# Performance work log

Measured on AMD Instinct MI355X. Metric: run time of the kernel, lower is better.

Reference implementation:

```python
import jax, jax.numpy as jnp
import numpy as np

B, N, C, H = 16, 4096, 1024, 8
D = C // H  # head dim = 128
EPS = 1e-5


def layernorm(x, gamma, beta):
    mu = jnp.mean(x, axis=-1, keepdims=True)
    var = jnp.mean(jnp.square(x - mu), axis=-1, keepdims=True)
    return (x - mu) * jax.lax.rsqrt(var + EPS) * gamma + beta


def setup_inputs() -> dict:
    key = jax.random.key(0)
    ks = jax.random.split(key, 5)
    w_std = C ** -0.5
    return {
        "class_feature": jax.random.normal(ks[0], (1, 1, C), dtype=jnp.float32),
        "features": jax.random.normal(ks[1], (B, N, C), dtype=jnp.float32),
        "q_gamma": jnp.ones((C,), jnp.float32),
        "q_beta": jnp.zeros((C,), jnp.float32),
        "Wq": jax.random.normal(ks[2], (C, C), dtype=jnp.float32) * w_std,
        "kv_gamma": jnp.ones((C,), jnp.float32),
        "kv_beta": jnp.zeros((C,), jnp.float32),
        "Wkv": jax.random.normal(ks[3], (2 * C, C), dtype=jnp.float32) * w_std,
        "proj_W": jax.random.normal(ks[4], (C, C), dtype=jnp.float32) * w_std,
        "proj_b": jnp.zeros((C,), jnp.float32),
    }


def reference(class_feature, features, q_gamma, q_beta, Wq,
              kv_gamma, kv_beta, Wkv, proj_W, proj_b):
    b, n, c = features.shape
    scale = c ** -0.5  # NOTE: original scales by input_size^-0.5, not head_dim^-0.5
    cf = jnp.broadcast_to(class_feature, (b, 1, c))  # repeat(B,1,1)

    # q branch: LN + Linear (no bias); single query token per batch
    q = layernorm(cf, q_gamma, q_beta) @ Wq.T            # (B,1,C)
    q = q.reshape(b, H, D)                               # (B,H,D)

    # kv branch: LN + Linear -> split into k,v per head
    kv = layernorm(features, kv_gamma, kv_beta) @ Wkv.T  # (B,N,2C)
    kv = kv.reshape(b, n, 2, H, D)
    k = kv[:, :, 0]                                      # (B,N,H,D)
    v = kv[:, :, 1]                                      # (B,N,H,D)

    # single-query attention per head
    attn = jnp.einsum('bhd,bnhd->bhn', q * scale, k)     # (B,H,N)
    attn = jax.nn.softmax(attn, axis=-1)
    agg = jnp.einsum('bhn,bnhd->bhd', attn, v)           # (B,H,D)
    agg = agg.reshape(b, 1, c)

    return cf + agg @ proj_W.T + proj_b
```

## Files before the change

### kernel.cpp

```cpp
#include <hip/hip_runtime.h>
#include <math.h>


#define BB 16
#define NN 4096
#define CC 1024
#define HH 8
#define DD 128
#define CHUNKS 64
#define RPB 64
#define TPT 4
#define NT 16

constexpr float EPS_ = 1e-5f;
constexpr float SCALE_ = 0.03125f;

__device__ __forceinline__ float wsum(float v) {
#pragma unroll
  for (int o = 32; o; o >>= 1) v += __shfl_xor(v, o, 64);
  return v;
}

__device__ __forceinline__ float dpp_sum63(float v) {
  int t;
  t = __builtin_amdgcn_update_dpp(0, __float_as_int(v), 0x111, 0xf, 0xf, true);  v += __int_as_float(t);
  t = __builtin_amdgcn_update_dpp(0, __float_as_int(v), 0x112, 0xf, 0xf, true);  v += __int_as_float(t);
  t = __builtin_amdgcn_update_dpp(0, __float_as_int(v), 0x114, 0xf, 0xf, true);  v += __int_as_float(t);
  t = __builtin_amdgcn_update_dpp(0, __float_as_int(v), 0x118, 0xf, 0xf, true);  v += __int_as_float(t);
  t = __builtin_amdgcn_update_dpp(0, __float_as_int(v), 0x142, 0xa, 0xf, false); v += __int_as_float(t);
  t = __builtin_amdgcn_update_dpp(0, __float_as_int(v), 0x143, 0xc, 0xf, false); v += __int_as_float(t);
  return v;
}

__device__ __forceinline__ float rsum_u(float v) {
  return __int_as_float(__builtin_amdgcn_readlane(__float_as_int(dpp_sum63(v)), 63));
}

__device__ __forceinline__ float dot4(const float4& a, const float4& b) {
  return a.x * b.x + a.y * b.y + a.z * b.z + a.w * b.w;
}
__device__ __forceinline__ void fma4(float4& a, float s, const float4& v) {
  a.x += s * v.x; a.y += s * v.y; a.z += s * v.z; a.w += s * v.w;
}

__device__ __forceinline__ void bar_lgkm() {
  asm volatile("s_waitcnt lgkmcnt(0)" ::: "memory");
  __builtin_amdgcn_sched_barrier(0);
  __builtin_amdgcn_s_barrier();
  __builtin_amdgcn_sched_barrier(0);
}

__global__ __launch_bounds__(256) void k0b(const float* __restrict__ cf,
                                           const float* __restrict__ g,
                                           const float* __restrict__ be,
                                           const float* __restrict__ Wq,
                                           float* __restrict__ qvec) {
  __shared__ __align__(16) float lnbuf[CC];
  __shared__ float red[8];
  int t = threadIdx.x, lane = t & 63, wid = t >> 6;
  float x[4];
  float s = 0.f, s2 = 0.f;
#pragma unroll
  for (int j = 0; j < 4; ++j) {
    x[j] = cf[t * 4 + j];
    s += x[j];
    s2 += x[j] * x[j];
  }
  s = wsum(s);
  s2 = wsum(s2);
  if (lane == 0) { red[wid] = s; red[4 + wid] = s2; }
  __syncthreads();
  float S = red[0] + red[1] + red[2] + red[3];
  float S2 = red[4] + red[5] + red[6] + red[7];
  float mu = S * (1.f / CC);
  float rstd = rsqrtf(S2 * (1.f / CC) - mu * mu + EPS_);
#pragma unroll
  for (int j = 0; j < 4; ++j)
    lnbuf[t * 4 + j] = (x[j] - mu) * rstd * g[t * 4 + j] + be[t * 4 + j];
  __syncthreads();
  int j = blockIdx.x * 4 + wid;
  const float4* wr = (const float4*)(Wq + (size_t)j * CC);
  const float4* l4 = (const float4*)lnbuf;
  float a = 0.f;
#pragma unroll
  for (int k = 0; k < 4; ++k) a += dot4(wr[lane + 64 * k], l4[lane + 64 * k]);
  a = wsum(a);
  if (lane == 0) qvec[j] = a;
}

__global__ __launch_bounds__(256) void k0c(const float* __restrict__ qvec,
                                           const float* __restrict__ Wkv,
                                           const float* __restrict__ kvg,
                                           float* __restrict__ qW,
                                           float* __restrict__ qWg) {
  int h = blockIdx.x >> 4;
  int c0 = (blockIdx.x & 15) * 64;
  int t = threadIdx.x, cl = t & 63, g = t >> 6;
  float a = 0.f;
#pragma unroll 8
  for (int d = g * 32; d < g * 32 + 32; ++d)
    a += qvec[h * DD + d] * Wkv[((size_t)(h * DD + d)) * CC + c0 + cl];
  __shared__ float red[4][64];
  red[g][cl] = a;
  __syncthreads();
  if (t < 64) {
    float v = (red[0][t] + red[1][t] + red[2][t] + red[3][t]) * SCALE_;
    qW[h * CC + c0 + t] = v;
    qWg[h * CC + c0 + t] = v * kvg[c0 + t];
  }
}

__global__ __launch_bounds__(256, 2) void kfused(
    const float* __restrict__ x, const float* __restrict__ qWg,
    const float* __restrict__ qW, const float* __restrict__ kvb,
    float* __restrict__ part_s, float* __restrict__ part_meu) {
  __shared__ __align__(16) float xbuf[2][TPT * CC];
  __shared__ __align__(8) float mr_lds[2][TPT][2];

  const int t = threadIdx.x, lane = t & 63, wid = t >> 6;
  const int chunk = blockIdx.x, b = blockIdx.y;
  const int bc = b * CHUNKS + chunk;
  const int h0 = wid * 2;

  const float* gx = x + ((size_t)b * NN + (size_t)chunk * RPB) * CC;
  const int sl = wid * 256 + lane;

  float4 pf[4];
  {
    const float4* g0 = (const float4*)gx;
#pragma unroll
    for (int k = 0; k < 4; ++k) pf[k] = g0[sl + 64 * k];
  }

  float4 qw0[4], qw1[4];
  {
    const float4* a0 = (const float4*)(qWg + (size_t)h0 * CC);
    const float4* a1 = (const float4*)(qWg + (size_t)(h0 + 1) * CC);
#pragma unroll
    for (int k = 0; k < 4; ++k) {
      qw0[k] = a0[lane + 64 * k];
      qw1[k] = a1[lane + 64 * k];
    }
  }
  float qs0, qs1, qb0, qb1;
  {
    float s0 = 0.f, s1 = 0.f, t0 = 0.f, t1 = 0.f;
    const float4* w0 = (const float4*)(qW + (size_t)h0 * CC);
    const float4* w1 = (const float4*)(qW + (size_t)(h0 + 1) * CC);
    const float4* b4 = (const float4*)kvb;
#pragma unroll
    for (int k = 0; k < 4; ++k) {
      s0 += qw0[k].x + qw0[k].y + qw0[k].z + qw0[k].w;
      s1 += qw1[k].x + qw1[k].y + qw1[k].z + qw1[k].w;
      float4 bt = b4[lane + 64 * k];
      t0 += dot4(w0[lane + 64 * k], bt);
      t1 += dot4(w1[lane + 64 * k], bt);
    }
    qs0 = rsum_u(s0);
    qs1 = rsum_u(s1);
    qb0 = rsum_u(t0);
    qb1 = rsum_u(t1);
  }

  float4 acc0[4], acc1[4];
#pragma unroll
  for (int k = 0; k < 4; ++k) {
    acc0[k] = make_float4(0.f, 0.f, 0.f, 0.f);
    acc1[k] = make_float4(0.f, 0.f, 0.f, 0.f);
  }
  float e0 = 0.f, e1 = 0.f, un0 = 0.f, un1 = 0.f;

  for (int tl = 0; tl < NT; ++tl) {
    const int cur = tl & 1;
    float ls = 0.f, ls2 = 0.f;
#pragma unroll
    for (int k = 0; k < 4; ++k) {
      ls += pf[k].x + pf[k].y + pf[k].z + pf[k].w;
      ls2 += dot4(pf[k], pf[k]);
    }
    {
      float4* dst = (float4*)xbuf[cur];
#pragma unroll
      for (int k = 0; k < 4; ++k) dst[sl + 64 * k] = pf[k];
    }
    ls = dpp_sum63(ls);
    ls2 = dpp_sum63(ls2);
    if (lane == 63) {
      float mu = ls * (1.f / CC);
      float rs = rsqrtf(ls2 * (1.f / CC) - mu * mu + EPS_);
      mr_lds[cur][wid][0] = mu;
      mr_lds[cur][wid][1] = rs;
    }
    if (tl + 1 < NT) {
      const float4* gn = (const float4*)(gx + (size_t)(tl + 1) * (TPT * CC));
#pragma unroll
      for (int k = 0; k < 4; ++k) pf[k] = gn[sl + 64 * k];
    }
    bar_lgkm();

    const float4* xb4 = (const float4*)xbuf[cur];
#pragma unroll
    for (int r = 0; r < TPT; ++r) {
      float4 x0 = xb4[r * 256 + lane];
      float4 x1 = xb4[r * 256 + lane + 64];
      float4 x2 = xb4[r * 256 + lane + 128];
      float4 x3 = xb4[r * 256 + lane + 192];
      float a0 = dot4(qw0[0], x0), a1 = dot4(qw0[1], x1);
      float a2 = dot4(qw0[2], x2), a3 = dot4(qw0[3], x3);
      float c0 = dot4(qw1[0], x0), c1 = dot4(qw1[1], x1);
      float c2 = dot4(qw1[2], x2), c3 = dot4(qw1[3], x3);
      float D0 = rsum_u((a0 + a1) + (a2 + a3));
      float D1 = rsum_u((c0 + c1) + (c2 + c3));
      float2 mr = *(const float2*)mr_lds[cur][r];
      float mu = mr.x, rs = mr.y;
      float l0 = fminf(rs * (D0 - mu * qs0) + qb0, 75.f);
      float l1 = fminf(rs * (D1 - mu * qs1) + qb1, 75.f);
      float p0 = __expf(l0), p1 = __expf(l1);
      float w0 = p0 * rs, w1 = p1 * rs;
      e0 += p0; e1 += p1;
      un0 += w0 * mu; un1 += w1 * mu;
      fma4(acc0[0], w0, x0); fma4(acc0[1], w0, x1);
      fma4(acc0[2], w0, x2); fma4(acc0[3], w0, x3);
      fma4(acc1[0], w1, x0); fma4(acc1[1], w1, x1);
      fma4(acc1[2], w1, x2); fma4(acc1[3], w1, x3);
    }
  }

  float4* p0 = (float4*)(part_s + ((size_t)bc * HH + h0) * CC);
  float4* p1 = (float4*)(part_s + ((size_t)bc * HH + h0 + 1) * CC);
#pragma unroll
  for (int k = 0; k < 4; ++k) {
    p0[64 * k + lane] = acc0[k];
    p1[64 * k + lane] = acc1[k];
  }
  if (lane == 0) {
    float* pm = part_meu + ((size_t)bc * HH + h0) * 3;
    pm[0] = 0.f; pm[1] = e0; pm[2] = un0;
    pm[3] = 0.f; pm[4] = e1; pm[5] = un1;
  }
}

__global__ __launch_bounds__(256) void kmerge(
    const float* __restrict__ part_s, const float* __restrict__ part_meu,
    const float* __restrict__ kvg, const float* __restrict__ kvb,
    float* __restrict__ s) {
  int h = blockIdx.x >> 2, q = blockIdx.x & 3, b = blockIdx.y;
  int col = q * 256 + threadIdx.x;
  float E = 0.f, UN = 0.f, a = 0.f;
  for (int ch = 0; ch < CHUNKS; ++ch) {
    const float* pm = part_meu + (((size_t)b * CHUNKS + ch) * HH + h) * 3;
    E += pm[1];
    UN += pm[2];
    a += part_s[(((size_t)b * CHUNKS + ch) * HH + h) * CC + col];
  }
  float inv = 1.f / E;
  s[((size_t)b * HH + h) * CC + col] = kvg[col] * (a - UN) * inv + kvb[col];
}

__global__ __launch_bounds__(256) void k5(const float* __restrict__ Wkv,
                                          const float* __restrict__ s,
                                          float* __restrict__ agg) {
  int lane = threadIdx.x & 63;
  int j = blockIdx.x * 4 + (threadIdx.x >> 6);
  int h = j >> 7;
  const float4* wr = (const float4*)(Wkv + ((size_t)(CC + j)) * CC);
  float4 wv[4];
#pragma unroll
  for (int k = 0; k < 4; ++k) wv[k] = wr[lane + 64 * k];
  for (int b = 0; b < BB; ++b) {
    const float4* s4 = (const float4*)(s + ((size_t)(b * HH + h)) * CC);
    float a = 0.f;
#pragma unroll
    for (int k = 0; k < 4; ++k) a += dot4(wv[k], s4[lane + 64 * k]);
    a = wsum(a);
    if (lane == 0) agg[b * CC + j] = a;
  }
}

__global__ __launch_bounds__(256) void k6(const float* __restrict__ pW,
                                          const float* __restrict__ agg,
                                          const float* __restrict__ cf,
                                          const float* __restrict__ pb,
                                          float* __restrict__ out) {
  int lane = threadIdx.x & 63;
  int j = blockIdx.x * 4 + (threadIdx.x >> 6);
  const float4* wr = (const float4*)(pW + (size_t)j * CC);
  float4 wv[4];
#pragma unroll
  for (int k = 0; k < 4; ++k) wv[k] = wr[lane + 64 * k];
  for (int b = 0; b < BB; ++b) {
    const float4* a4 = (const float4*)(agg + (size_t)b * CC);
    float a = 0.f;
#pragma unroll
    for (int k = 0; k < 4; ++k) a += dot4(wv[k], a4[lane + 64 * k]);
    a = wsum(a);
    if (lane == 0) out[b * CC + j] = cf[j] + a + pb[j];
  }
}

constexpr size_t WS_QVEC = 0;
constexpr size_t WS_QW   = 1024;
constexpr size_t WS_QWG  = 9216;
constexpr size_t WS_S    = 17408;
constexpr size_t WS_AGG  = 148480;
constexpr size_t WS_PMEU = 164864;
constexpr size_t WS_PART = 189440;

extern "C" void kernel_launch(void* const* d_in, const int* in_sizes, int n_in,
                              void* d_out, int out_size, void* d_ws, size_t ws_size,
                              hipStream_t stream) {
  const float* cf = (const float*)d_in[0];
  const float* x = (const float*)d_in[1];
  const float* qg = (const float*)d_in[2];
  const float* qb = (const float*)d_in[3];
  const float* Wq = (const float*)d_in[4];
  const float* kvg = (const float*)d_in[5];
  const float* kvb = (const float*)d_in[6];
  const float* Wkv = (const float*)d_in[7];
  const float* pW = (const float*)d_in[8];
  const float* pb = (const float*)d_in[9];
  float* ws = (float*)d_ws;
  float* out = (float*)d_out;

  k0b<<<256, 256, 0, stream>>>(cf, qg, qb, Wq, ws + WS_QVEC);
  k0c<<<128, 256, 0, stream>>>(ws + WS_QVEC, Wkv, kvg, ws + WS_QW, ws + WS_QWG);
  kfused<<<dim3(CHUNKS, BB), 256, 0, stream>>>(x, ws + WS_QWG, ws + WS_QW, kvb,
                                               ws + WS_PART, ws + WS_PMEU);
  kmerge<<<dim3(HH * 4, BB), 256, 0, stream>>>(ws + WS_PART, ws + WS_PMEU, kvg, kvb,
                                               ws + WS_S);
  k5<<<256, 256, 0, stream>>>(Wkv, ws + WS_S, ws + WS_AGG);
  k6<<<256, 256, 0, stream>>>(pW, ws + WS_AGG, cf, pb, out);
}
```

Baseline: 114.1 us.

## Double rows per tile in fused kernel, halving chunk count and partials

Raises rows per tile from 4 to 8 so each wave loads and normalizes two rows per iteration. Halving the chunk count halves the partial sums written and merged, and the per-chunk meta record shrinks from three floats to two. The larger shared tile (64KB per block) and the doubled prefetch registers may cut occupancy. Halving the block count (512 blocks) can also leave CUs underused.

```diff
diff --git a/kernel.cpp b/kernel.cpp
--- a/kernel.cpp
+++ b/kernel.cpp
@@ -7,9 +7,9 @@
 #define CC 1024
 #define HH 8
 #define DD 128
-#define CHUNKS 64
-#define RPB 64
-#define TPT 4
+#define CHUNKS 32
+#define RPB 128
+#define TPT 8
 #define NT 16
 
 constexpr float EPS_ = 1e-5f;
@@ -38,6 +38,9 @@
 
 __device__ __forceinline__ float dot4(const float4& a, const float4& b) {
   return a.x * b.x + a.y * b.y + a.z * b.z + a.w * b.w;
+}
+__device__ __forceinline__ float sum4(const float4& a) {
+  return (a.x + a.y) + (a.z + a.w);
 }
 __device__ __forceinline__ void fma4(float4& a, float s, const float4& v) {
   a.x += s * v.x; a.y += s * v.y; a.z += s * v.z; a.w += s * v.w;
@@ -121,15 +124,18 @@
   const int chunk = blockIdx.x, b = blockIdx.y;
   const int bc = b * CHUNKS + chunk;
   const int h0 = wid * 2;
+  const int ra = wid * 2, rb = ra + 1;
 
   const float* gx = x + ((size_t)b * NN + (size_t)chunk * RPB) * CC;
-  const int sl = wid * 256 + lane;
-
-  float4 pf[4];
+
+  float4 pf[8];
   {
     const float4* g0 = (const float4*)gx;
 #pragma unroll
-    for (int k = 0; k < 4; ++k) pf[k] = g0[sl + 64 * k];
+    for (int k = 0; k < 4; ++k) {
+      pf[k] = g0[ra * 256 + lane + 64 * k];
+      pf[4 + k] = g0[rb * 256 + lane + 64 * k];
+    }
   }
 
   float4 qw0[4], qw1[4];
@@ -150,8 +156,8 @@
     const float4* b4 = (const float4*)kvb;
 #pragma unroll
     for (int k = 0; k < 4; ++k) {
-      s0 += qw0[k].x + qw0[k].y + qw0[k].z + qw0[k].w;
-      s1 += qw1[k].x + qw1[k].y + qw1[k].z + qw1[k].w;
+      s0 += sum4(qw0[k]);
+      s1 += sum4(qw1[k]);
       float4 bt = b4[lane + 64 * k];
       t0 += dot4(w0[lane + 64 * k], bt);
       t1 += dot4(w1[lane + 64 * k], bt);
@@ -172,29 +178,44 @@
 
   for (int tl = 0; tl < NT; ++tl) {
     const int cur = tl & 1;
-    float ls = 0.f, ls2 = 0.f;
+
+    float lsA = 0.f, lsA2 = 0.f, lsB = 0.f, lsB2 = 0.f;
 #pragma unroll
     for (int k = 0; k < 4; ++k) {
-      ls += pf[k].x + pf[k].y + pf[k].z + pf[k].w;
-      ls2 += dot4(pf[k], pf[k]);
+      lsA += sum4(pf[k]);
+      lsA2 += dot4(pf[k], pf[k]);
+      lsB += sum4(pf[4 + k]);
+      lsB2 += dot4(pf[4 + k], pf[4 + k]);
     }
     {
       float4* dst = (float4*)xbuf[cur];
 #pragma unroll
-      for (int k = 0; k < 4; ++k) dst[sl + 64 * k] = pf[k];
-    }
-    ls = dpp_sum63(ls);
-    ls2 = dpp_sum63(ls2);
+      for (int k = 0; k < 4; ++k) {
+        dst[ra * 256 + lane + 64 * k] = pf[k];
+        dst[rb * 256 + lane + 64 * k] = pf[4 + k];
+      }
+    }
+    lsA = dpp_sum63(lsA);
+    lsA2 = dpp_sum63(lsA2);
+    lsB = dpp_sum63(lsB);
+    lsB2 = dpp_sum63(lsB2);
     if (lane == 63) {
-      float mu = ls * (1.f / CC);
-      float rs = rsqrtf(ls2 * (1.f / CC) - mu * mu + EPS_);
-      mr_lds[cur][wid][0] = mu;
-      mr_lds[cur][wid][1] = rs;
+      float muA = lsA * (1.f / CC);
+      float rsA = rsqrtf(lsA2 * (1.f / CC) - muA * muA + EPS_);
+      float muB = lsB * (1.f / CC);
+      float rsB = rsqrtf(lsB2 * (1.f / CC) - muB * muB + EPS_);
+      mr_lds[cur][ra][0] = muA;
+      mr_lds[cur][ra][1] = rsA;
+      mr_lds[cur][rb][0] = muB;
+      mr_lds[cur][rb][1] = rsB;
     }
     if (tl + 1 < NT) {
       const float4* gn = (const float4*)(gx + (size_t)(tl + 1) * (TPT * CC));
 #pragma unroll
-      for (int k = 0; k < 4; ++k) pf[k] = gn[sl + 64 * k];
+      for (int k = 0; k < 4; ++k) {
+        pf[k] = gn[ra * 256 + lane + 64 * k];
+        pf[4 + k] = gn[rb * 256 + lane + 64 * k];
+      }
     }
     bar_lgkm();
 
@@ -234,9 +255,9 @@
     p1[64 * k + lane] = acc1[k];
   }
   if (lane == 0) {
-    float* pm = part_meu + ((size_t)bc * HH + h0) * 3;
-    pm[0] = 0.f; pm[1] = e0; pm[2] = un0;
-    pm[3] = 0.f; pm[4] = e1; pm[5] = un1;
+    float* pm = part_meu + ((size_t)bc * HH + h0) * 2;
+    pm[0] = e0; pm[1] = un0;
+    pm[2] = e1; pm[3] = un1;
   }
 }
 
@@ -248,9 +269,9 @@
   int col = q * 256 + threadIdx.x;
   float E = 0.f, UN = 0.f, a = 0.f;
   for (int ch = 0; ch < CHUNKS; ++ch) {
-    const float* pm = part_meu + (((size_t)b * CHUNKS + ch) * HH + h) * 3;
-    E += pm[1];
-    UN += pm[2];
+    const float* pm = part_meu + (((size_t)b * CHUNKS + ch) * HH + h) * 2;
+    E += pm[0];
+    UN += pm[1];
     a += part_s[(((size_t)b * CHUNKS + ch) * HH + h) * CC + col];
   }
   float inv = 1.f / E;
@@ -304,7 +325,7 @@
 constexpr size_t WS_S    = 17408;
 constexpr size_t WS_AGG  = 148480;
 constexpr size_t WS_PMEU = 164864;
-constexpr size_t WS_PART = 189440;
+constexpr size_t WS_PART = 173056;
 
 extern "C" void kernel_launch(void* const* d_in, const int* in_sizes, int n_in,
                               void* d_out, int out_size, void* d_ws, size_t ws_size,
```

Result: slower. 229.9 us (+101.5%).

## Use packed FP32 FMAs in attention loop and halve chunk count

Applied to the files above, without the earlier changes.

The main streaming kernel now does its dot products, LayerNorm statistics and weighted accumulation with v_pk_fma_f32/v_pk_add_f32 inline asm on float pairs, which is meant to halve the VALU instruction count per row. Rows per block double and the chunk count halves, so there are fewer partial results for the merge kernel to reduce. The per-chunk metadata also drops from three floats to two. The cost is fewer blocks in flight, less latency hiding, and inline asm that limits compiler scheduling.

```diff
diff --git a/kernel.cpp b/kernel.cpp
--- a/kernel.cpp
+++ b/kernel.cpp
@@ -7,13 +7,24 @@
 #define CC 1024
 #define HH 8
 #define DD 128
-#define CHUNKS 64
-#define RPB 64
+#define CHUNKS 32
+#define RPB 128
 #define TPT 4
-#define NT 16
+#define NT 32
 
 constexpr float EPS_ = 1e-5f;
 constexpr float SCALE_ = 0.03125f;
+
+typedef float v2f __attribute__((ext_vector_type(2)));
+
+__device__ __forceinline__ void pkfma(v2f& d, v2f a, v2f b) {
+  asm("v_pk_fma_f32 %0, %1, %2, %0" : "+v"(d) : "v"(a), "v"(b));
+}
+__device__ __forceinline__ void pkadd(v2f& d, v2f a) {
+  asm("v_pk_add_f32 %0, %1, %0" : "+v"(d) : "v"(a));
+}
+__device__ __forceinline__ v2f lo2(const float4& f) { return v2f{f.x, f.y}; }
+__device__ __forceinline__ v2f hi2(const float4& f) { return v2f{f.z, f.w}; }
 
 __device__ __forceinline__ float wsum(float v) {
 #pragma unroll
@@ -39,8 +50,8 @@
 __device__ __forceinline__ float dot4(const float4& a, const float4& b) {
   return a.x * b.x + a.y * b.y + a.z * b.z + a.w * b.w;
 }
-__device__ __forceinline__ void fma4(float4& a, float s, const float4& v) {
-  a.x += s * v.x; a.y += s * v.y; a.z += s * v.z; a.w += s * v.w;
+__device__ __forceinline__ float sum4(const float4& a) {
+  return (a.x + a.y) + (a.z + a.w);
 }
 
 __device__ __forceinline__ void bar_lgkm() {
@@ -150,8 +161,8 @@
     const float4* b4 = (const float4*)kvb;
 #pragma unroll
     for (int k = 0; k < 4; ++k) {
-      s0 += qw0[k].x + qw0[k].y + qw0[k].z + qw0[k].w;
-      s1 += qw1[k].x + qw1[k].y + qw1[k].z + qw1[k].w;
+      s0 += sum4(qw0[k]);
+      s1 += sum4(qw1[k]);
       float4 bt = b4[lane + 64 * k];
       t0 += dot4(w0[lane + 64 * k], bt);
       t1 += dot4(w1[lane + 64 * k], bt);
@@ -162,34 +173,41 @@
     qb1 = rsum_u(t1);
   }
 
-  float4 acc0[4], acc1[4];
-#pragma unroll
-  for (int k = 0; k < 4; ++k) {
-    acc0[k] = make_float4(0.f, 0.f, 0.f, 0.f);
-    acc1[k] = make_float4(0.f, 0.f, 0.f, 0.f);
+  v2f acc0[8], acc1[8];
+#pragma unroll
+  for (int k = 0; k < 8; ++k) {
+    acc0[k] = v2f{0.f, 0.f};
+    acc1[k] = v2f{0.f, 0.f};
   }
   float e0 = 0.f, e1 = 0.f, un0 = 0.f, un1 = 0.f;
 
   for (int tl = 0; tl < NT; ++tl) {
     const int cur = tl & 1;
-    float ls = 0.f, ls2 = 0.f;
-#pragma unroll
-    for (int k = 0; k < 4; ++k) {
-      ls += pf[k].x + pf[k].y + pf[k].z + pf[k].w;
-      ls2 += dot4(pf[k], pf[k]);
-    }
     {
-      float4* dst = (float4*)xbuf[cur];
-#pragma unroll
-      for (int k = 0; k < 4; ++k) dst[sl + 64 * k] = pf[k];
-    }
-    ls = dpp_sum63(ls);
-    ls2 = dpp_sum63(ls2);
-    if (lane == 63) {
-      float mu = ls * (1.f / CC);
-      float rs = rsqrtf(ls2 * (1.f / CC) - mu * mu + EPS_);
-      mr_lds[cur][wid][0] = mu;
-      mr_lds[cur][wid][1] = rs;
+      v2f sv = v2f{0.f, 0.f}, sv2 = v2f{0.f, 0.f};
+#pragma unroll
+      for (int k = 0; k < 4; ++k) {
+        v2f plo = lo2(pf[k]), phi = hi2(pf[k]);
+        pkadd(sv, plo);
+        pkadd(sv, phi);
+        pkfma(sv2, plo, plo);
+        pkfma(sv2, phi, phi);
+      }
+      float ls = sv.x + sv.y;
+      float ls2 = sv2.x + sv2.y;
+      {
+        float4* dst = (float4*)xbuf[cur];
+#pragma unroll
+        for (int k = 0; k < 4; ++k) dst[sl + 64 * k] = pf[k];
+      }
+      ls = dpp_sum63(ls);
+      ls2 = dpp_sum63(ls2);
+      if (lane == 63) {
+        float mu = ls * (1.f / CC);
+        float rs = rsqrtf(ls2 * (1.f / CC) - mu * mu + EPS_);
+        mr_lds[cur][wid][0] = mu;
+        mr_lds[cur][wid][1] = rs;
+      }
     }
     if (tl + 1 < NT) {
       const float4* gn = (const float4*)(gx + (size_t)(tl + 1) * (TPT * CC));
@@ -205,12 +223,19 @@
       float4 x1 = xb4[r * 256 + lane + 64];
       float4 x2 = xb4[r * 256 + lane + 128];
       float4 x3 = xb4[r * 256 + lane + 192];
-      float a0 = dot4(qw0[0], x0), a1 = dot4(qw0[1], x1);
-      float a2 = dot4(qw0[2], x2), a3 = dot4(qw0[3], x3);
-      float c0 = dot4(qw1[0], x0), c1 = dot4(qw1[1], x1);
-      float c2 = dot4(qw1[2], x2), c3 = dot4(qw1[3], x3);
-      float D0 = rsum_u((a0 + a1) + (a2 + a3));
-      float D1 = rsum_u((c0 + c1) + (c2 + c3));
+      v2f xl0 = lo2(x0), xh0 = hi2(x0), xl1 = lo2(x1), xh1 = hi2(x1);
+      v2f xl2 = lo2(x2), xh2 = hi2(x2), xl3 = lo2(x3), xh3 = hi2(x3);
+      v2f d0v = v2f{0.f, 0.f}, d1v = v2f{0.f, 0.f};
+      pkfma(d0v, lo2(qw0[0]), xl0); pkfma(d0v, hi2(qw0[0]), xh0);
+      pkfma(d0v, lo2(qw0[1]), xl1); pkfma(d0v, hi2(qw0[1]), xh1);
+      pkfma(d0v, lo2(qw0[2]), xl2); pkfma(d0v, hi2(qw0[2]), xh2);
+      pkfma(d0v, lo2(qw0[3]), xl3); pkfma(d0v, hi2(qw0[3]), xh3);
+      pkfma(d1v, lo2(qw1[0]), xl0); pkfma(d1v, hi2(qw1[0]), xh0);
+      pkfma(d1v, lo2(qw1[1]), xl1); pkfma(d1v, hi2(qw1[1]), xh1);
+      pkfma(d1v, lo2(qw1[2]), xl2); pkfma(d1v, hi2(qw1[2]), xh2);
+      pkfma(d1v, lo2(qw1[3]), xl3); pkfma(d1v, hi2(qw1[3]), xh3);
+      float D0 = rsum_u(d0v.x + d0v.y);
+      float D1 = rsum_u(d1v.x + d1v.y);
       float2 mr = *(const float2*)mr_lds[cur][r];
       float mu = mr.x, rs = mr.y;
       float l0 = fminf(rs * (D0 - mu * qs0) + qb0, 75.f);
@@ -219,10 +244,15 @@
       float w0 = p0 * rs, w1 = p1 * rs;
       e0 += p0; e1 += p1;
       un0 += w0 * mu; un1 += w1 * mu;
-      fma4(acc0[0], w0, x0); fma4(acc0[1], w0, x1);
-      fma4(acc0[2], w0, x2); fma4(acc0[3], w0, x3);
-      fma4(acc1[0], w1, x0); fma4(acc1[1], w1, x1);
-      fma4(acc1[2], w1, x2); fma4(acc1[3], w1, x3);
+      v2f w0v = v2f{w0, w0}, w1v = v2f{w1, w1};
+      pkfma(acc0[0], w0v, xl0); pkfma(acc0[1], w0v, xh0);
+      pkfma(acc0[2], w0v, xl1); pkfma(acc0[3], w0v, xh1);
+      pkfma(acc0[4], w0v, xl2); pkfma(acc0[5], w0v, xh2);
+      pkfma(acc0[6], w0v, xl3); pkfma(acc0[7], w0v, xh3);
+      pkfma(acc1[0], w1v, xl0); pkfma(acc1[1], w1v, xh0);
+      pkfma(acc1[2], w1v, xl1); pkfma(acc1[3], w1v, xh1);
+      pkfma(acc1[4], w1v, xl2); pkfma(acc1[5], w1v, xh2);
+      pkfma(acc1[6], w1v, xl3); pkfma(acc1[7], w1v, xh3);
     }
   }
 
@@ -230,13 +260,15 @@
   float4* p1 = (float4*)(part_s + ((size_t)bc * HH + h0 + 1) * CC);
 #pragma unroll
   for (int k = 0; k < 4; ++k) {
-    p0[64 * k + lane] = acc0[k];
-    p1[64 * k + lane] = acc1[k];
+    p0[64 * k + lane] = make_float4(acc0[2 * k].x, acc0[2 * k].y,
+                                    acc0[2 * k + 1].x, acc0[2 * k + 1].y);
+    p1[64 * k + lane] = make_float4(acc1[2 * k].x, acc1[2 * k].y,
+                                    acc1[2 * k + 1].x, acc1[2 * k + 1].y);
   }
   if (lane == 0) {
-    float* pm = part_meu + ((size_t)bc * HH + h0) * 3;
-    pm[0] = 0.f; pm[1] = e0; pm[2] = un0;
-    pm[3] = 0.f; pm[4] = e1; pm[5] = un1;
+    float* pm = part_meu + ((size_t)bc * HH + h0) * 2;
+    pm[0] = e0; pm[1] = un0;
+    pm[2] = e1; pm[3] = un1;
   }
 }
 
@@ -248,9 +280,9 @@
   int col = q * 256 + threadIdx.x;
   float E = 0.f, UN = 0.f, a = 0.f;
   for (int ch = 0; ch < CHUNKS; ++ch) {
-    const float* pm = part_meu + (((size_t)b * CHUNKS + ch) * HH + h) * 3;
-    E += pm[1];
-    UN += pm[2];
+    const float* pm = part_meu + (((size_t)b * CHUNKS + ch) * HH + h) * 2;
+    E += pm[0];
+    UN += pm[1];
     a += part_s[(((size_t)b * CHUNKS + ch) * HH + h) * CC + col];
   }
   float inv = 1.f / E;
@@ -304,7 +336,7 @@
 constexpr size_t WS_S    = 17408;
 constexpr size_t WS_AGG  = 148480;
 constexpr size_t WS_PMEU = 164864;
-constexpr size_t WS_PART = 189440;
+constexpr size_t WS_PART = 173056;
 
 extern "C" void kernel_launch(void* const* d_in, const int* in_sizes, int n_in,
                               void* d_out, int out_size, void* d_ws, size_t ws_size,
```

Measured after the change: 102.4 us, median of 2. -10.3%, faster.
